# Kernel optimization log

Measured on AMD Instinct MI355X. Metric: run time of the kernel, lower is better.

## Reference

```python
import jax, jax.numpy as jnp
import numpy as np

B, IN, H, L = 4096, 1024, 1024, 8


def setup_inputs() -> dict:
    key = jax.random.key(0)
    k1, k2, k3, k4, k5 = jax.random.split(key, 5)
    scale = 0.02
    inputs = jax.random.normal(k1, (B, IN), dtype=jnp.float32)
    # Stacked gate weights, order [f, i, o, g] along first axis (torch Linear: y = x @ W.T + b)
    W = jax.random.normal(k2, (4 * H, IN), dtype=jnp.float32) * scale   # input->gates
    bW = jax.random.normal(k3, (4 * H,), dtype=jnp.float32) * scale
    U = jax.random.normal(k4, (4 * H, H), dtype=jnp.float32) * scale    # hidden->gates
    bU = jax.random.normal(k5, (4 * H,), dtype=jnp.float32) * scale
    return {"inputs": inputs, "W": W, "bW": bW, "U": U, "bU": bU, "num_layers": L}


def reference(inputs, W, bW, U, bU, num_layers):
    batch = inputs.shape[0]
    hid = U.shape[1]
    # Input projection is loop-invariant: compute once. [B, 4H]
    x_proj = jnp.einsum('bi,gi->bg', inputs, W) + bW
    xf, xi, xo, xg = jnp.split(x_proj, 4, axis=1)

    def step(carry, _):
        ht, ct = carry
        h_proj = jnp.einsum('bh,gh->bg', ht, U) + bU  # [B, 4H]
        hf, hi, ho, hg = jnp.split(h_proj, 4, axis=1)
        f = jax.nn.sigmoid(xf + hf)
        i = jax.nn.sigmoid(xi + hi)
        o = jax.nn.sigmoid(xo + ho)
        g = jnp.tanh(xg + hg)
        ct_new = f * ct + i * g
        ht_new = o * jnp.tanh(ct_new)
        return (ht_new, ct_new), None

    h0 = jnp.zeros((batch, hid), dtype=inputs.dtype)
    c0 = jnp.zeros((batch, hid), dtype=inputs.dtype)
    (ht, ct), _ = jax.lax.scan(step, (h0, c0), None, length=num_layers)
    return ht, ct
```

## Files before the change

### kernel.cpp

```cpp
#include <hip/hip_runtime.h>
#include <hip/hip_bf16.h>

typedef __bf16 bf16x8 __attribute__((ext_vector_type(8)));
typedef float f32x4 __attribute__((ext_vector_type(4)));

#define DEVI static __device__ __forceinline__

DEVI void load_lds16(const void* g, void* l) {
  __builtin_amdgcn_global_load_lds(
      (const __attribute__((address_space(1))) void*)g,
      (__attribute__((address_space(3))) void*)l, 16, 0, 0);
}

DEVI unsigned short f2b(float f) { return __bfloat16_as_ushort(__float2bfloat16(f)); }
DEVI float b2f(unsigned short u) {
  union { unsigned int i; float f; } c;
  c.i = ((unsigned int)u) << 16;
  return c.f;
}
DEVI float sigm(float x) { return 1.0f / (1.0f + __expf(-x)); }
DEVI float tanh_fast(float x) { return 2.0f / (1.0f + __expf(-2.0f * x)) - 1.0f; }

DEVI int swz(int L) { return L ^ (((L >> 7) & 7) << 4); }

__global__ __launch_bounds__(256) void cast_kernel(const float* __restrict__ src,
                                                   unsigned short* __restrict__ dst,
                                                   int n4) {
  const int i = blockIdx.x * 256 + threadIdx.x;
  if (i >= n4) return;
  const float4 v = reinterpret_cast<const float4*>(src)[i];
  ushort4 o;
  o.x = f2b(v.x); o.y = f2b(v.y); o.z = f2b(v.z); o.w = f2b(v.w);
  reinterpret_cast<ushort4*>(dst)[i] = o;
}

__global__ __launch_bounds__(256) void cast_perm_kernel(const float* __restrict__ src,
                                                        unsigned short* __restrict__ dst) {
  const int i = blockIdx.x * 256 + threadIdx.x;
  const int r = i >> 8;
  const int cw = i & 255;
  const float4 v = reinterpret_cast<const float4*>(src)[i];
  const int rp = ((r & 1023) << 2) + (r >> 10);
  ushort4 o;
  o.x = f2b(v.x); o.y = f2b(v.y); o.z = f2b(v.z); o.w = f2b(v.w);
  *reinterpret_cast<ushort4*>(&dst[(size_t)rp * 1024 + (cw << 2)]) = o;
}

__global__ __launch_bounds__(256) void bias_prep(const float* __restrict__ bW,
                                                 const float* __restrict__ bU,
                                                 float* __restrict__ bp) {
  const int i = blockIdx.x * 256 + threadIdx.x;
  const int h = i >> 2, g = i & 3;
  bp[i] = bW[g * 1024 + h] + bU[g * 1024 + h];
}

template <int MODE>
__global__ __launch_bounds__(512, 2) void gemm256(
    const unsigned short* __restrict__ A,
    const unsigned short* __restrict__ Bm,
    const unsigned short* __restrict__ xpb_r,
    unsigned short* __restrict__ xpb_w,
    const float* __restrict__ bp,
    unsigned short* __restrict__ ct,
    unsigned short* __restrict__ htout,
    float* __restrict__ out) {
  constexpr int K = 1024, N = 4096;
  constexpr int NPH = K / 32;
  __shared__ unsigned char lds[256 * 528];

  const int tid = threadIdx.x;
  const int lane = tid & 63;
  const int wave = tid >> 6;
  const int wr = wave >> 2;
  const int wc = wave & 3;

  const int bid = blockIdx.x;
  const int sw = (bid & 7) * 32 + (bid >> 3);
  const int brow = (sw >> 4) * 256;
  const int bcol = (sw & 15) * 256;

  const int physA0 = tid * 16;
  const int physA1 = 8192 + tid * 16;
  const int physB0 = 16384 + tid * 16;
  const int physB1 = 24576 + tid * 16;
  const int LA0 = swz(physA0), LA1 = swz(physA1);
  const int LB0 = swz(physB0 - 16384), LB1 = swz(physB1 - 16384);
  const unsigned char* pA0 = (const unsigned char*)A + (size_t)(brow + (LA0 >> 6)) * (K * 2) + (LA0 & 63);
  const unsigned char* pA1 = (const unsigned char*)A + (size_t)(brow + (LA1 >> 6)) * (K * 2) + (LA1 & 63);
  const unsigned char* pB0 = (const unsigned char*)Bm + (size_t)(bcol + (LB0 >> 6)) * (K * 2) + (LB0 & 63);
  const unsigned char* pB1 = (const unsigned char*)Bm + (size_t)(bcol + (LB1 >> 6)) * (K * 2) + (LB1 & 63);

  const int s16 = (lane >> 4) * 16;
  int offA[8], offB[4];
#pragma unroll
  for (int m = 0; m < 8; ++m) {
    const int row = wr * 128 + m * 16 + (lane & 15);
    offA[m] = swz(row * 64 + s16);
  }
#pragma unroll
  for (int n = 0; n < 4; ++n) {
    const int row = wc * 64 + n * 16 + (lane & 15);
    offB[n] = 16384 + swz(row * 64 + s16);
  }

  f32x4 acc[8][4] = {};

  auto STAGE = [&](int q) {
    unsigned char* sb = lds + (q & 3) * 32768;
    const size_t kb = (size_t)q * 64;
    load_lds16(pA0 + kb, sb + physA0);
    load_lds16(pA1 + kb, sb + physA1);
    load_lds16(pB0 + kb, sb + physB0);
    load_lds16(pB1 + kb, sb + physB1);
  };

  STAGE(0); STAGE(1); STAGE(2);
  asm volatile("s_waitcnt vmcnt(8)" ::: "memory");
  __builtin_amdgcn_s_barrier();
  __builtin_amdgcn_sched_barrier(0);

  for (int p = 0; p < NPH; ++p) {
    if (p + 3 < NPH) STAGE(p + 3);

    const unsigned char* sl = lds + (p & 3) * 32768;
    bf16x8 af[8], bf[4];
#pragma unroll
    for (int n = 0; n < 4; ++n) bf[n] = *reinterpret_cast<const bf16x8*>(sl + offB[n]);
#pragma unroll
    for (int m = 0; m < 8; ++m) af[m] = *reinterpret_cast<const bf16x8*>(sl + offA[m]);

    __builtin_amdgcn_s_setprio(1);
#pragma unroll
    for (int m = 0; m < 8; ++m)
#pragma unroll
      for (int n = 0; n < 4; ++n)
        acc[m][n] = __builtin_amdgcn_mfma_f32_16x16x32_bf16(af[m], bf[n], acc[m][n], 0, 0, 0);
    __builtin_amdgcn_s_setprio(0);

    if (p < NPH - 1) {
      if (p < NPH - 3)
        asm volatile("s_waitcnt vmcnt(8)" ::: "memory");
      else if (p == NPH - 3)
        asm volatile("s_waitcnt vmcnt(4)" ::: "memory");
      else
        asm volatile("s_waitcnt vmcnt(0)" ::: "memory");
      __builtin_amdgcn_s_barrier();
      __builtin_amdgcn_sched_barrier(0);
    }
  }

  __syncthreads();
  unsigned short* cs = (unsigned short*)lds;
  {
    const int c0 = wc * 64 + (lane & 15);
    const int r00 = wr * 128 + ((lane >> 4) << 2);
#pragma unroll
    for (int m = 0; m < 8; ++m)
#pragma unroll
      for (int n = 0; n < 4; ++n) {
        const int rr = r00 + m * 16;
        const int cc = c0 + n * 16;
#pragma unroll
        for (int r = 0; r < 4; ++r) cs[(rr + r) * 264 + cc] = f2b(acc[m][n][r]);
      }
  }
  __syncthreads();

  const int hbase = bcol >> 2;
#pragma unroll 4
  for (int j = 0; j < 32; ++j) {
    const int q = tid + (j << 9);
    const int row = q >> 6;
    const int hh = q & 63;
    const ushort4 pv = *reinterpret_cast<const ushort4*>(&cs[row * 264 + hh * 4]);
    const int ci = (brow + row) * 1024 + hbase + hh;
    float sf, si, so, sg;
    if constexpr (MODE == 0) {
      const float4 bpv = *reinterpret_cast<const float4*>(&bp[bcol + hh * 4]);
      sf = b2f(pv.x) + bpv.x;
      si = b2f(pv.y) + bpv.y;
      so = b2f(pv.z) + bpv.z;
      sg = b2f(pv.w) + bpv.w;
      ushort4 xo;
      xo.x = f2b(sf); xo.y = f2b(si); xo.z = f2b(so); xo.w = f2b(sg);
      *reinterpret_cast<ushort4*>(&xpb_w[(size_t)(brow + row) * N + bcol + hh * 4]) = xo;
    } else {
      const ushort4 xv = *reinterpret_cast<const ushort4*>(&xpb_r[(size_t)(brow + row) * N + bcol + hh * 4]);
      sf = b2f(pv.x) + b2f(xv.x);
      si = b2f(pv.y) + b2f(xv.y);
      so = b2f(pv.z) + b2f(xv.z);
      sg = b2f(pv.w) + b2f(xv.w);
    }
    const float c_old = (MODE == 0) ? 0.0f : b2f(ct[ci]);
    const float f = sigm(sf);
    const float ii = sigm(si);
    const float o = sigm(so);
    const float gg = tanh_fast(sg);
    const float c = fmaf(f, c_old, ii * gg);
    const float h = o * tanh_fast(c);
    if constexpr (MODE == 2) {
      out[ci] = h;
      out[4194304 + ci] = c;
    } else {
      ct[ci] = f2b(c);
      htout[ci] = f2b(h);
    }
  }
}

extern "C" void kernel_launch(void* const* d_in, const int* in_sizes, int n_in,
                              void* d_out, int out_size, void* d_ws, size_t ws_size,
                              hipStream_t stream) {
  const float* x = (const float*)d_in[0];
  const float* W = (const float*)d_in[1];
  const float* bW = (const float*)d_in[2];
  const float* U = (const float*)d_in[3];
  const float* bU = (const float*)d_in[4];
  float* out = (float*)d_out;

  char* w = (char*)d_ws;
  const size_t MB = 1ull << 20;
  unsigned short* xb = (unsigned short*)(w + 0 * MB);
  unsigned short* Wbp = (unsigned short*)(w + 8 * MB);
  unsigned short* Ubp = (unsigned short*)(w + 16 * MB);
  unsigned short* xpb = (unsigned short*)(w + 24 * MB);
  unsigned short* ct = (unsigned short*)(w + 56 * MB);
  unsigned short* htA = (unsigned short*)(w + 64 * MB);
  unsigned short* htB = (unsigned short*)(w + 72 * MB);
  float* bp = (float*)(w + 80 * MB);

  const int n4 = (4096 * 1024) / 4;
  cast_kernel<<<4096, 256, 0, stream>>>(x, xb, n4);
  cast_perm_kernel<<<4096, 256, 0, stream>>>(W, Wbp);
  cast_perm_kernel<<<4096, 256, 0, stream>>>(U, Ubp);
  bias_prep<<<16, 256, 0, stream>>>(bW, bU, bp);

  gemm256<0><<<256, 512, 0, stream>>>(xb, Wbp, nullptr, xpb, bp, ct, htA, nullptr);

  const unsigned short* hin = htA;
  unsigned short* hout = htB;
  for (int t = 1; t <= 6; ++t) {
    gemm256<1><<<256, 512, 0, stream>>>(hin, Ubp, xpb, nullptr, nullptr, ct, hout, nullptr);
    const unsigned short* tmp = hout;
    hout = (unsigned short*)hin;
    hin = tmp;
  }
  gemm256<2><<<256, 512, 0, stream>>>(hin, Ubp, xpb, nullptr, nullptr, ct, nullptr, out);
}
```

Before: 402.6 us.

## Fuse LSTM timesteps into one cooperative persistent kernel and merge prep kernels

Merges the four input-preparation kernels into a single launch, and replaces the eight per-timestep GEMM launches with one cooperative kernel that loops over timesteps and uses grid.sync between them. The aim is to remove kernel launch overhead and the tail gaps between dependent launches. In exchange it pays for a grid-wide barrier each step. It also depends on all 256 blocks of 512 threads being co-resident; cooperative launch fails if they cannot all fit.

```diff
diff --git a/kernel.cpp b/kernel.cpp
--- a/kernel.cpp
+++ b/kernel.cpp
@@ -1,5 +1,8 @@
 #include <hip/hip_runtime.h>
 #include <hip/hip_bf16.h>
+#include <hip/hip_cooperative_groups.h>
+
+namespace cg = cooperative_groups;
 
 typedef __bf16 bf16x8 __attribute__((ext_vector_type(8)));
 typedef float f32x4 __attribute__((ext_vector_type(4)));
@@ -23,47 +26,49 @@
 
 DEVI int swz(int L) { return L ^ (((L >> 7) & 7) << 4); }
 
-__global__ __launch_bounds__(256) void cast_kernel(const float* __restrict__ src,
-                                                   unsigned short* __restrict__ dst,
-                                                   int n4) {
-  const int i = blockIdx.x * 256 + threadIdx.x;
-  if (i >= n4) return;
-  const float4 v = reinterpret_cast<const float4*>(src)[i];
-  ushort4 o;
-  o.x = f2b(v.x); o.y = f2b(v.y); o.z = f2b(v.z); o.w = f2b(v.w);
-  reinterpret_cast<ushort4*>(dst)[i] = o;
-}
-
-__global__ __launch_bounds__(256) void cast_perm_kernel(const float* __restrict__ src,
-                                                        unsigned short* __restrict__ dst) {
-  const int i = blockIdx.x * 256 + threadIdx.x;
-  const int r = i >> 8;
-  const int cw = i & 255;
-  const float4 v = reinterpret_cast<const float4*>(src)[i];
-  const int rp = ((r & 1023) << 2) + (r >> 10);
-  ushort4 o;
-  o.x = f2b(v.x); o.y = f2b(v.y); o.z = f2b(v.z); o.w = f2b(v.w);
-  *reinterpret_cast<ushort4*>(&dst[(size_t)rp * 1024 + (cw << 2)]) = o;
-}
-
-__global__ __launch_bounds__(256) void bias_prep(const float* __restrict__ bW,
-                                                 const float* __restrict__ bU,
-                                                 float* __restrict__ bp) {
-  const int i = blockIdx.x * 256 + threadIdx.x;
-  const int h = i >> 2, g = i & 3;
-  bp[i] = bW[g * 1024 + h] + bU[g * 1024 + h];
-}
-
-template <int MODE>
-__global__ __launch_bounds__(512, 2) void gemm256(
-    const unsigned short* __restrict__ A,
-    const unsigned short* __restrict__ Bm,
-    const unsigned short* __restrict__ xpb_r,
-    unsigned short* __restrict__ xpb_w,
+__global__ __launch_bounds__(256) void prep_kernel(
+    const float* __restrict__ x, const float* __restrict__ W,
+    const float* __restrict__ U, const float* __restrict__ bW,
+    const float* __restrict__ bU, unsigned short* __restrict__ xb,
+    unsigned short* __restrict__ Wbp, unsigned short* __restrict__ Ubp,
+    float* __restrict__ bp) {
+  const int bid = blockIdx.x;
+  if (bid < 4096) {
+    const int i = bid * 256 + threadIdx.x;
+    const float4 v = reinterpret_cast<const float4*>(x)[i];
+    ushort4 o;
+    o.x = f2b(v.x); o.y = f2b(v.y); o.z = f2b(v.z); o.w = f2b(v.w);
+    reinterpret_cast<ushort4*>(xb)[i] = o;
+  } else if (bid < 12288) {
+    const bool isW = bid < 8192;
+    const float* src = isW ? W : U;
+    unsigned short* dst = isW ? Wbp : Ubp;
+    const int i = (bid - (isW ? 4096 : 8192)) * 256 + threadIdx.x;
+    const int r = i >> 8;
+    const int cw = i & 255;
+    const float4 v = reinterpret_cast<const float4*>(src)[i];
+    const int rp = ((r & 1023) << 2) + (r >> 10);
+    ushort4 o;
+    o.x = f2b(v.x); o.y = f2b(v.y); o.z = f2b(v.z); o.w = f2b(v.w);
+    *reinterpret_cast<ushort4*>(&dst[(size_t)rp * 1024 + (cw << 2)]) = o;
+  } else {
+    const int i = (bid - 12288) * 256 + threadIdx.x;
+    const int h = i >> 2, g = i & 3;
+    bp[i] = bW[g * 1024 + h] + bU[g * 1024 + h];
+  }
+}
+
+__global__ __launch_bounds__(512, 2) void lstm_all(
+    const unsigned short* __restrict__ xb,
+    const unsigned short* __restrict__ Wbp,
+    const unsigned short* __restrict__ Ubp,
+    unsigned short* __restrict__ xpb,
     const float* __restrict__ bp,
     unsigned short* __restrict__ ct,
-    unsigned short* __restrict__ htout,
+    unsigned short* __restrict__ htA,
+    unsigned short* __restrict__ htB,
     float* __restrict__ out) {
+  cg::grid_group grid = cg::this_grid();
   constexpr int K = 1024, N = 4096;
   constexpr int NPH = K / 32;
   __shared__ unsigned char lds[256 * 528];
@@ -85,10 +90,10 @@
   const int physB1 = 24576 + tid * 16;
   const int LA0 = swz(physA0), LA1 = swz(physA1);
   const int LB0 = swz(physB0 - 16384), LB1 = swz(physB1 - 16384);
-  const unsigned char* pA0 = (const unsigned char*)A + (size_t)(brow + (LA0 >> 6)) * (K * 2) + (LA0 & 63);
-  const unsigned char* pA1 = (const unsigned char*)A + (size_t)(brow + (LA1 >> 6)) * (K * 2) + (LA1 & 63);
-  const unsigned char* pB0 = (const unsigned char*)Bm + (size_t)(bcol + (LB0 >> 6)) * (K * 2) + (LB0 & 63);
-  const unsigned char* pB1 = (const unsigned char*)Bm + (size_t)(bcol + (LB1 >> 6)) * (K * 2) + (LB1 & 63);
+  const size_t goA0 = (size_t)(brow + (LA0 >> 6)) * (K * 2) + (LA0 & 63);
+  const size_t goA1 = (size_t)(brow + (LA1 >> 6)) * (K * 2) + (LA1 & 63);
+  const size_t goB0 = (size_t)(bcol + (LB0 >> 6)) * (K * 2) + (LB0 & 63);
+  const size_t goB1 = (size_t)(bcol + (LB1 >> 6)) * (K * 2) + (LB1 & 63);
 
   const int s16 = (lane >> 4) * 16;
   int offA[8], offB[4];
@@ -103,107 +108,149 @@
     offB[n] = 16384 + swz(row * 64 + s16);
   }
 
-  f32x4 acc[8][4] = {};
-
-  auto STAGE = [&](int q) {
-    unsigned char* sb = lds + (q & 3) * 32768;
-    const size_t kb = (size_t)q * 64;
-    load_lds16(pA0 + kb, sb + physA0);
-    load_lds16(pA1 + kb, sb + physA1);
-    load_lds16(pB0 + kb, sb + physB0);
-    load_lds16(pB1 + kb, sb + physB1);
-  };
-
-  STAGE(0); STAGE(1); STAGE(2);
-  asm volatile("s_waitcnt vmcnt(8)" ::: "memory");
-  __builtin_amdgcn_s_barrier();
-  __builtin_amdgcn_sched_barrier(0);
-
-  for (int p = 0; p < NPH; ++p) {
-    if (p + 3 < NPH) STAGE(p + 3);
-
-    const unsigned char* sl = lds + (p & 3) * 32768;
-    bf16x8 af[8], bf[4];
-#pragma unroll
-    for (int n = 0; n < 4; ++n) bf[n] = *reinterpret_cast<const bf16x8*>(sl + offB[n]);
-#pragma unroll
-    for (int m = 0; m < 8; ++m) af[m] = *reinterpret_cast<const bf16x8*>(sl + offA[m]);
-
-    __builtin_amdgcn_s_setprio(1);
-#pragma unroll
-    for (int m = 0; m < 8; ++m)
-#pragma unroll
-      for (int n = 0; n < 4; ++n)
-        acc[m][n] = __builtin_amdgcn_mfma_f32_16x16x32_bf16(af[m], bf[n], acc[m][n], 0, 0, 0);
-    __builtin_amdgcn_s_setprio(0);
-
-    if (p < NPH - 1) {
-      if (p < NPH - 3)
-        asm volatile("s_waitcnt vmcnt(8)" ::: "memory");
-      else if (p == NPH - 3)
-        asm volatile("s_waitcnt vmcnt(4)" ::: "memory");
-      else
-        asm volatile("s_waitcnt vmcnt(0)" ::: "memory");
-      __builtin_amdgcn_s_barrier();
-      __builtin_amdgcn_sched_barrier(0);
-    }
-  }
-
-  __syncthreads();
-  unsigned short* cs = (unsigned short*)lds;
-  {
-    const int c0 = wc * 64 + (lane & 15);
-    const int r00 = wr * 128 + ((lane >> 4) << 2);
-#pragma unroll
-    for (int m = 0; m < 8; ++m)
-#pragma unroll
-      for (int n = 0; n < 4; ++n) {
-        const int rr = r00 + m * 16;
-        const int cc = c0 + n * 16;
-#pragma unroll
-        for (int r = 0; r < 4; ++r) cs[(rr + r) * 264 + cc] = f2b(acc[m][n][r]);
-      }
-  }
-  __syncthreads();
-
   const int hbase = bcol >> 2;
+
+  for (int t = 0; t < 8; ++t) {
+    const unsigned short* Amat = (t == 0) ? xb : ((t & 1) ? htA : htB);
+    const unsigned short* Bmat = (t == 0) ? Wbp : Ubp;
+    unsigned short* hout = (t & 1) ? htB : htA;
+    const int mode = (t == 0) ? 0 : ((t == 7) ? 2 : 1);
+
+    const unsigned char* pA0 = (const unsigned char*)Amat + goA0;
+    const unsigned char* pA1 = (const unsigned char*)Amat + goA1;
+    const unsigned char* pB0 = (const unsigned char*)Bmat + goB0;
+    const unsigned char* pB1 = (const unsigned char*)Bmat + goB1;
+
+    f32x4 acc[8][4] = {};
+
+    auto STAGE = [&](int q) {
+      unsigned char* sb = lds + (q & 3) * 32768;
+      const size_t kb = (size_t)q * 64;
+      load_lds16(pA0 + kb, sb + physA0);
+      load_lds16(pA1 + kb, sb + physA1);
+      load_lds16(pB0 + kb, sb + physB0);
+      load_lds16(pB1 + kb, sb + physB1);
+    };
+
+    STAGE(0); STAGE(1); STAGE(2);
+    asm volatile("s_waitcnt vmcnt(8)" ::: "memory");
+    __builtin_amdgcn_s_barrier();
+    __builtin_amdgcn_sched_barrier(0);
+
+    for (int p = 0; p < NPH; ++p) {
+      if (p + 3 < NPH) STAGE(p + 3);
+
+      const unsigned char* sl = lds + (p & 3) * 32768;
+      bf16x8 af[8], bf[4];
+#pragma unroll
+      for (int n = 0; n < 4; ++n) bf[n] = *reinterpret_cast<const bf16x8*>(sl + offB[n]);
+#pragma unroll
+      for (int m = 0; m < 8; ++m) af[m] = *reinterpret_cast<const bf16x8*>(sl + offA[m]);
+
+      __builtin_amdgcn_s_setprio(1);
+#pragma unroll
+      for (int m = 0; m < 8; ++m)
+#pragma unroll
+        for (int n = 0; n < 4; ++n)
+          acc[m][n] = __builtin_amdgcn_mfma_f32_16x16x32_bf16(af[m], bf[n], acc[m][n], 0, 0, 0);
+      __builtin_amdgcn_s_setprio(0);
+
+      if (p < NPH - 1) {
+        if (p < NPH - 3)
+          asm volatile("s_waitcnt vmcnt(8)" ::: "memory");
+        else if (p == NPH - 3)
+          asm volatile("s_waitcnt vmcnt(4)" ::: "memory");
+        else
+          asm volatile("s_waitcnt vmcnt(0)" ::: "memory");
+        __builtin_amdgcn_s_barrier();
+        __builtin_amdgcn_sched_barrier(0);
+      }
+    }
+
+    __syncthreads();
+    unsigned short* cs = (unsigned short*)lds;
+    {
+      const int c0 = wc * 64 + (lane & 15);
+      const int r00 = wr * 128 + ((lane >> 4) << 2);
+#pragma unroll
+      for (int m = 0; m < 8; ++m)
+#pragma unroll
+        for (int n = 0; n < 4; ++n) {
+          const int rr = r00 + m * 16;
+          const int cc = c0 + n * 16;
+#pragma unroll
+          for (int r = 0; r < 4; ++r) cs[(rr + r) * 264 + cc] = f2b(acc[m][n][r]);
+        }
+    }
+    __syncthreads();
+
+    if (mode == 0) {
 #pragma unroll 4
-  for (int j = 0; j < 32; ++j) {
-    const int q = tid + (j << 9);
-    const int row = q >> 6;
-    const int hh = q & 63;
-    const ushort4 pv = *reinterpret_cast<const ushort4*>(&cs[row * 264 + hh * 4]);
-    const int ci = (brow + row) * 1024 + hbase + hh;
-    float sf, si, so, sg;
-    if constexpr (MODE == 0) {
-      const float4 bpv = *reinterpret_cast<const float4*>(&bp[bcol + hh * 4]);
-      sf = b2f(pv.x) + bpv.x;
-      si = b2f(pv.y) + bpv.y;
-      so = b2f(pv.z) + bpv.z;
-      sg = b2f(pv.w) + bpv.w;
-      ushort4 xo;
-      xo.x = f2b(sf); xo.y = f2b(si); xo.z = f2b(so); xo.w = f2b(sg);
-      *reinterpret_cast<ushort4*>(&xpb_w[(size_t)(brow + row) * N + bcol + hh * 4]) = xo;
+      for (int j = 0; j < 32; ++j) {
+        const int q = tid + (j << 9);
+        const int row = q >> 6;
+        const int hh = q & 63;
+        const ushort4 pv = *reinterpret_cast<const ushort4*>(&cs[row * 264 + hh * 4]);
+        const float4 bpv = *reinterpret_cast<const float4*>(&bp[bcol + hh * 4]);
+        const int ci = (brow + row) * 1024 + hbase + hh;
+        const float sf = b2f(pv.x) + bpv.x;
+        const float si = b2f(pv.y) + bpv.y;
+        const float so = b2f(pv.z) + bpv.z;
+        const float sg = b2f(pv.w) + bpv.w;
+        ushort4 xo;
+        xo.x = f2b(sf); xo.y = f2b(si); xo.z = f2b(so); xo.w = f2b(sg);
+        *reinterpret_cast<ushort4*>(&xpb[(size_t)(brow + row) * N + bcol + hh * 4]) = xo;
+        const float ii = sigm(si);
+        const float o = sigm(so);
+        const float gg = tanh_fast(sg);
+        const float c = ii * gg;
+        const float h = o * tanh_fast(c);
+        ct[ci] = f2b(c);
+        hout[ci] = f2b(h);
+      }
+    } else if (mode == 1) {
+#pragma unroll 4
+      for (int j = 0; j < 32; ++j) {
+        const int q = tid + (j << 9);
+        const int row = q >> 6;
+        const int hh = q & 63;
+        const ushort4 pv = *reinterpret_cast<const ushort4*>(&cs[row * 264 + hh * 4]);
+        const ushort4 xv = *reinterpret_cast<const ushort4*>(&xpb[(size_t)(brow + row) * N + bcol + hh * 4]);
+        const int ci = (brow + row) * 1024 + hbase + hh;
+        const float c_old = b2f(ct[ci]);
+        const float f = sigm(b2f(pv.x) + b2f(xv.x));
+        const float ii = sigm(b2f(pv.y) + b2f(xv.y));
+        const float o = sigm(b2f(pv.z) + b2f(xv.z));
+        const float gg = tanh_fast(b2f(pv.w) + b2f(xv.w));
+        const float c = fmaf(f, c_old, ii * gg);
+        const float h = o * tanh_fast(c);
+        ct[ci] = f2b(c);
+        hout[ci] = f2b(h);
+      }
     } else {
-      const ushort4 xv = *reinterpret_cast<const ushort4*>(&xpb_r[(size_t)(brow + row) * N + bcol + hh * 4]);
-      sf = b2f(pv.x) + b2f(xv.x);
-      si = b2f(pv.y) + b2f(xv.y);
-      so = b2f(pv.z) + b2f(xv.z);
-      sg = b2f(pv.w) + b2f(xv.w);
-    }
-    const float c_old = (MODE == 0) ? 0.0f : b2f(ct[ci]);
-    const float f = sigm(sf);
-    const float ii = sigm(si);
-    const float o = sigm(so);
-    const float gg = tanh_fast(sg);
-    const float c = fmaf(f, c_old, ii * gg);
-    const float h = o * tanh_fast(c);
-    if constexpr (MODE == 2) {
-      out[ci] = h;
-      out[4194304 + ci] = c;
-    } else {
-      ct[ci] = f2b(c);
-      htout[ci] = f2b(h);
+#pragma unroll 4
+      for (int j = 0; j < 32; ++j) {
+        const int q = tid + (j << 9);
+        const int row = q >> 6;
+        const int hh = q & 63;
+        const ushort4 pv = *reinterpret_cast<const ushort4*>(&cs[row * 264 + hh * 4]);
+        const ushort4 xv = *reinterpret_cast<const ushort4*>(&xpb[(size_t)(brow + row) * N + bcol + hh * 4]);
+        const int ci = (brow + row) * 1024 + hbase + hh;
+        const float c_old = b2f(ct[ci]);
+        const float f = sigm(b2f(pv.x) + b2f(xv.x));
+        const float ii = sigm(b2f(pv.y) + b2f(xv.y));
+        const float o = sigm(b2f(pv.z) + b2f(xv.z));
+        const float gg = tanh_fast(b2f(pv.w) + b2f(xv.w));
+        const float c = fmaf(f, c_old, ii * gg);
+        const float h = o * tanh_fast(c);
+        out[ci] = h;
+        out[4194304 + ci] = c;
+      }
+    }
+
+    if (t < 7) {
+      asm volatile("s_waitcnt vmcnt(0)" ::: "memory");
+      grid.sync();
     }
   }
 }
@@ -229,21 +276,9 @@
   unsigned short* htB = (unsigned short*)(w + 72 * MB);
   float* bp = (float*)(w + 80 * MB);
 
-  const int n4 = (4096 * 1024) / 4;
-  cast_kernel<<<4096, 256, 0, stream>>>(x, xb, n4);
-  cast_perm_kernel<<<4096, 256, 0, stream>>>(W, Wbp);
-  cast_perm_kernel<<<4096, 256, 0, stream>>>(U, Ubp);
-  bias_prep<<<16, 256, 0, stream>>>(bW, bU, bp);
-
-  gemm256<0><<<256, 512, 0, stream>>>(xb, Wbp, nullptr, xpb, bp, ct, htA, nullptr);
-
-  const unsigned short* hin = htA;
-  unsigned short* hout = htB;
-  for (int t = 1; t <= 6; ++t) {
-    gemm256<1><<<256, 512, 0, stream>>>(hin, Ubp, xpb, nullptr, nullptr, ct, hout, nullptr);
-    const unsigned short* tmp = hout;
-    hout = (unsigned short*)hin;
-    hin = tmp;
-  }
-  gemm256<2><<<256, 512, 0, stream>>>(hin, Ubp, xpb, nullptr, nullptr, ct, nullptr, out);
-}
+  prep_kernel<<<12304, 256, 0, stream>>>(x, W, U, bW, bU, xb, Wbp, Ubp, bp);
+
+  void* args[] = {(void*)&xb, (void*)&Wbp, (void*)&Ubp, (void*)&xpb, (void*)&bp,
+                  (void*)&ct, (void*)&htA, (void*)&htB, (void*)&out};
+  hipLaunchCooperativeKernel((const void*)lstm_all, dim3(256), dim3(512), args, 0, stream);
+}
```

Measured after the change: 577.7 us. +43.5%, slower.

## Software-pipeline LDS fragment loads with MFMAs and fuse prep kernels

Applied to the files above, without the earlier changes.

The GEMM main loop now double-buffers the B register fragments and loads the next phase's A/B fragments from LDS while issuing the current phase's MFMAs. Prefetch depth rises to four stages, so it relies on correct buffer reuse across the 4-slot ring. Separately, the three cast kernels and the bias prep are merged into one launch to cut launch overhead. The interleaving raises register pressure and adds tricky wait/barrier ordering that could introduce races.

```diff
diff --git a/kernel.cpp b/kernel.cpp
--- a/kernel.cpp
+++ b/kernel.cpp
@@ -23,36 +23,59 @@
 
 DEVI int swz(int L) { return L ^ (((L >> 7) & 7) << 4); }
 
-__global__ __launch_bounds__(256) void cast_kernel(const float* __restrict__ src,
-                                                   unsigned short* __restrict__ dst,
-                                                   int n4) {
-  const int i = blockIdx.x * 256 + threadIdx.x;
-  if (i >= n4) return;
-  const float4 v = reinterpret_cast<const float4*>(src)[i];
-  ushort4 o;
-  o.x = f2b(v.x); o.y = f2b(v.y); o.z = f2b(v.z); o.w = f2b(v.w);
-  reinterpret_cast<ushort4*>(dst)[i] = o;
-}
-
-__global__ __launch_bounds__(256) void cast_perm_kernel(const float* __restrict__ src,
-                                                        unsigned short* __restrict__ dst) {
-  const int i = blockIdx.x * 256 + threadIdx.x;
-  const int r = i >> 8;
-  const int cw = i & 255;
-  const float4 v = reinterpret_cast<const float4*>(src)[i];
-  const int rp = ((r & 1023) << 2) + (r >> 10);
-  ushort4 o;
-  o.x = f2b(v.x); o.y = f2b(v.y); o.z = f2b(v.z); o.w = f2b(v.w);
-  *reinterpret_cast<ushort4*>(&dst[(size_t)rp * 1024 + (cw << 2)]) = o;
-}
-
-__global__ __launch_bounds__(256) void bias_prep(const float* __restrict__ bW,
-                                                 const float* __restrict__ bU,
-                                                 float* __restrict__ bp) {
-  const int i = blockIdx.x * 256 + threadIdx.x;
-  const int h = i >> 2, g = i & 3;
-  bp[i] = bW[g * 1024 + h] + bU[g * 1024 + h];
-}
+__global__ __launch_bounds__(256) void prep_kernel(
+    const float* __restrict__ x, const float* __restrict__ W,
+    const float* __restrict__ U, const float* __restrict__ bW,
+    const float* __restrict__ bU, unsigned short* __restrict__ xb,
+    unsigned short* __restrict__ Wbp, unsigned short* __restrict__ Ubp,
+    float* __restrict__ bp) {
+  const int bid = blockIdx.x;
+  if (bid < 4096) {
+    const int i = bid * 256 + threadIdx.x;
+    const float4 v = reinterpret_cast<const float4*>(x)[i];
+    ushort4 o;
+    o.x = f2b(v.x); o.y = f2b(v.y); o.z = f2b(v.z); o.w = f2b(v.w);
+    reinterpret_cast<ushort4*>(xb)[i] = o;
+  } else if (bid < 12288) {
+    const bool isW = bid < 8192;
+    const float* src = isW ? W : U;
+    unsigned short* dst = isW ? Wbp : Ubp;
+    const int i = (bid - (isW ? 4096 : 8192)) * 256 + threadIdx.x;
+    const int r = i >> 8;
+    const int cw = i & 255;
+    const float4 v = reinterpret_cast<const float4*>(src)[i];
+    const int rp = ((r & 1023) << 2) + (r >> 10);
+    ushort4 o;
+    o.x = f2b(v.x); o.y = f2b(v.y); o.z = f2b(v.z); o.w = f2b(v.w);
+    *reinterpret_cast<ushort4*>(&dst[(size_t)rp * 1024 + (cw << 2)]) = o;
+  } else {
+    const int i = (bid - 12288) * 256 + threadIdx.x;
+    const int h = i >> 2, g = i & 3;
+    bp[i] = bW[g * 1024 + h] + bU[g * 1024 + h];
+  }
+}
+
+#define KPHASE(BFC, BFN, SLNXT, STAGEQ, DOSTAGE, WAITSTR, DOBAR)              \
+  {                                                                           \
+    if (DOSTAGE) STAGE(STAGEQ);                                               \
+    const unsigned char* sln_ = (SLNXT);                                      \
+    _Pragma("unroll") for (int n_ = 0; n_ < 4; ++n_)                          \
+        BFN[n_] = *reinterpret_cast<const bf16x8*>(sln_ + offB[n_]);          \
+    __builtin_amdgcn_s_setprio(1);                                            \
+    _Pragma("unroll") for (int m_ = 0; m_ < 8; ++m_) {                        \
+      _Pragma("unroll") for (int n_ = 0; n_ < 4; ++n_)                        \
+          acc[m_][n_] = __builtin_amdgcn_mfma_f32_16x16x32_bf16(              \
+              af[m_], BFC[n_], acc[m_][n_], 0, 0, 0);                         \
+      af[m_] = *reinterpret_cast<const bf16x8*>(sln_ + offA[m_]);             \
+    }                                                                         \
+    __builtin_amdgcn_s_setprio(0);                                            \
+    asm volatile(WAITSTR ::: "memory");                                       \
+    __builtin_amdgcn_sched_barrier(0);                                        \
+    if (DOBAR) {                                                              \
+      __builtin_amdgcn_s_barrier();                                           \
+      __builtin_amdgcn_sched_barrier(0);                                      \
+    }                                                                         \
+  }
 
 template <int MODE>
 __global__ __launch_bounds__(512, 2) void gemm256(
@@ -65,7 +88,6 @@
     unsigned short* __restrict__ htout,
     float* __restrict__ out) {
   constexpr int K = 1024, N = 4096;
-  constexpr int NPH = K / 32;
   __shared__ unsigned char lds[256 * 528];
 
   const int tid = threadIdx.x;
@@ -104,6 +126,7 @@
   }
 
   f32x4 acc[8][4] = {};
+  bf16x8 af[8], bfE[4], bfO[4];
 
   auto STAGE = [&](int q) {
     unsigned char* sb = lds + (q & 3) * 32768;
@@ -114,40 +137,35 @@
     load_lds16(pB1 + kb, sb + physB1);
   };
 
-  STAGE(0); STAGE(1); STAGE(2);
+  STAGE(0); STAGE(1); STAGE(2); STAGE(3);
   asm volatile("s_waitcnt vmcnt(8)" ::: "memory");
   __builtin_amdgcn_s_barrier();
+#pragma unroll
+  for (int n = 0; n < 4; ++n) bfE[n] = *reinterpret_cast<const bf16x8*>(lds + offB[n]);
+#pragma unroll
+  for (int m = 0; m < 8; ++m) af[m] = *reinterpret_cast<const bf16x8*>(lds + offA[m]);
+  asm volatile("s_waitcnt lgkmcnt(0)" ::: "memory");
   __builtin_amdgcn_sched_barrier(0);
-
-  for (int p = 0; p < NPH; ++p) {
-    if (p + 3 < NPH) STAGE(p + 3);
-
-    const unsigned char* sl = lds + (p & 3) * 32768;
-    bf16x8 af[8], bf[4];
-#pragma unroll
-    for (int n = 0; n < 4; ++n) bf[n] = *reinterpret_cast<const bf16x8*>(sl + offB[n]);
-#pragma unroll
-    for (int m = 0; m < 8; ++m) af[m] = *reinterpret_cast<const bf16x8*>(sl + offA[m]);
-
-    __builtin_amdgcn_s_setprio(1);
-#pragma unroll
-    for (int m = 0; m < 8; ++m)
-#pragma unroll
-      for (int n = 0; n < 4; ++n)
-        acc[m][n] = __builtin_amdgcn_mfma_f32_16x16x32_bf16(af[m], bf[n], acc[m][n], 0, 0, 0);
-    __builtin_amdgcn_s_setprio(0);
-
-    if (p < NPH - 1) {
-      if (p < NPH - 3)
-        asm volatile("s_waitcnt vmcnt(8)" ::: "memory");
-      else if (p == NPH - 3)
-        asm volatile("s_waitcnt vmcnt(4)" ::: "memory");
-      else
-        asm volatile("s_waitcnt vmcnt(0)" ::: "memory");
-      __builtin_amdgcn_s_barrier();
-      __builtin_amdgcn_sched_barrier(0);
-    }
-  }
+  __builtin_amdgcn_s_barrier();
+  __builtin_amdgcn_sched_barrier(0);
+
+  for (int pp = 0; pp < 14; ++pp) {
+    const int p = 2 * pp;
+    const unsigned char* sl1 = lds + ((p + 1) & 3) * 32768;
+    const unsigned char* sl2 = lds + ((p + 2) & 3) * 32768;
+    KPHASE(bfE, bfO, sl1, p + 4, true, "s_waitcnt vmcnt(8) lgkmcnt(0)", true);
+    KPHASE(bfO, bfE, sl2, p + 5, true, "s_waitcnt vmcnt(8) lgkmcnt(0)", true);
+  }
+  KPHASE(bfE, bfO, lds + (29 & 3) * 32768, 0, false, "s_waitcnt vmcnt(4) lgkmcnt(0)", true);
+  KPHASE(bfO, bfE, lds + (30 & 3) * 32768, 0, false, "s_waitcnt vmcnt(0) lgkmcnt(0)", true);
+  KPHASE(bfE, bfO, lds + (31 & 3) * 32768, 0, false, "s_waitcnt lgkmcnt(0)", false);
+  __builtin_amdgcn_s_setprio(1);
+#pragma unroll
+  for (int m = 0; m < 8; ++m)
+#pragma unroll
+    for (int n = 0; n < 4; ++n)
+      acc[m][n] = __builtin_amdgcn_mfma_f32_16x16x32_bf16(af[m], bfO[n], acc[m][n], 0, 0, 0);
+  __builtin_amdgcn_s_setprio(0);
 
   __syncthreads();
   unsigned short* cs = (unsigned short*)lds;
@@ -229,11 +247,7 @@
   unsigned short* htB = (unsigned short*)(w + 72 * MB);
   float* bp = (float*)(w + 80 * MB);
 
-  const int n4 = (4096 * 1024) / 4;
-  cast_kernel<<<4096, 256, 0, stream>>>(x, xb, n4);
-  cast_perm_kernel<<<4096, 256, 0, stream>>>(W, Wbp);
-  cast_perm_kernel<<<4096, 256, 0, stream>>>(U, Ubp);
-  bias_prep<<<16, 256, 0, stream>>>(bW, bU, bp);
+  prep_kernel<<<12304, 256, 0, stream>>>(x, W, U, bW, bU, xb, Wbp, Ubp, bp);
 
   gemm256<0><<<256, 512, 0, stream>>>(xb, Wbp, nullptr, xpb, bp, ct, htA, nullptr);
 
```

Result: faster. 387.4 us (-3.8%).
